# Optimization experiments

Measured on AMD Instinct MI355X. Metric: run time of the kernel, lower is better.

Reference implementation:

```python
import jax, jax.numpy as jnp
import numpy as np

NUM_HEADS = 16
HEAD_SIZE = 64
D_MODEL = NUM_HEADS * HEAD_SIZE  # 1024


def setup_inputs() -> dict:
    key = jax.random.key(0)
    k_in, k_ctx, k_q, k_k, k_v, k_o, k_b = jax.random.split(key, 7)
    B, Sq, Skv, D = 4, 2048, 2048, D_MODEL
    inputs = jax.random.normal(k_in, (B, Sq, D), dtype=jnp.float32)
    context = jax.random.normal(k_ctx, (B, Skv, D), dtype=jnp.float32)
    s = 0.02
    Wq = jax.random.normal(k_q, (D, D), dtype=jnp.float32) * s
    Wk = jax.random.normal(k_k, (D, D), dtype=jnp.float32) * s
    Wv = jax.random.normal(k_v, (D, D), dtype=jnp.float32) * s
    Wo = jax.random.normal(k_o, (D, D), dtype=jnp.float32) * s
    bo = jnp.zeros((D,), dtype=jnp.float32)
    return {"inputs": inputs, "context": context, "Wq": Wq, "Wk": Wk,
            "Wv": Wv, "Wo": Wo, "bo": bo}


def reference(inputs, context, Wq, Wk, Wv, Wo, bo):
    # inputs: [B, Sq, D]; context: [B, Skv, D]
    B, Sq, _ = inputs.shape
    H, Dh = NUM_HEADS, HEAD_SIZE
    scale = Dh ** -0.5
    q = (inputs @ Wq).reshape(B, Sq, H, Dh)          # [B,Sq,H,Dh]
    k = (context @ Wk).reshape(B, -1, H, Dh)          # [B,Skv,H,Dh]
    v = (context @ Wv).reshape(B, -1, H, Dh)
    # The chunked online-softmax recurrence in the source is exactly softmax attention.
    scores = jnp.einsum('bqhd,bkhd->bhqk', q, k) * scale
    probs = jax.nn.softmax(scores, axis=-1)
    attn = jnp.einsum('bhqk,bkhd->bqhd', probs, v)    # [B,Sq,H,Dh]
    out = attn.reshape(B, Sq, H * Dh)
    return out @ Wo + bo
```

## Files before the change

kernel.cpp:

```cpp
#include <hip/hip_runtime.h>
#include <hip/hip_bf16.h>


#define D_MODEL 1024
#define NHEAD   16
#define DHEAD   64
#define BATCH   4
#define SEQ     2048
#define MROWS   (BATCH * SEQ)
#define WP      ((size_t)D_MODEL * D_MODEL)

typedef unsigned short u16;
typedef __attribute__((ext_vector_type(8))) _Float16       f16x8;
typedef __attribute__((ext_vector_type(2))) _Float16       f16x2;
typedef __attribute__((ext_vector_type(4))) float          f32x4;
typedef __attribute__((ext_vector_type(8))) unsigned short u16x8;
typedef __attribute__((ext_vector_type(4))) unsigned short u16x4;

__device__ __forceinline__ u16 f2h(float x) {
    union { _Float16 h; u16 u; } cv;
    cv.h = (_Float16)x;
    return cv.u;
}

__device__ __forceinline__ unsigned pkrtz(float a, float b) {
    unsigned r;
    asm("v_cvt_pkrtz_f16_f32 %0, %1, %2" : "=v"(r) : "v"(a), "v"(b));
    return r;
}

__device__ __forceinline__ f32x4 mfma16h(f16x8 a, f16x8 b, f32x4 c) {
    return __builtin_amdgcn_mfma_f32_16x16x32_f16(a, b, c, 0, 0, 0);
}

__device__ __forceinline__ float exp2fast(float x) {
    float r;
    asm("v_exp_f32 %0, %1" : "=v"(r) : "v"(x));
    return r;
}

__device__ __forceinline__ void glds16(const void* g, void* l) {
    __builtin_amdgcn_global_load_lds(
        (const __attribute__((address_space(1))) void*)g,
        (__attribute__((address_space(3))) void*)l, 16, 0, 0);
}

__global__ __launch_bounds__(256) void cvt16(const float* __restrict__ a,
                                             const float* __restrict__ b,
                                             u16* __restrict__ oa,
                                             u16* __restrict__ ob) {
    const size_t i = ((size_t)blockIdx.x * 256 + threadIdx.x) * 8;
    {
        float4 v0 = *(const float4*)(a + i);
        float4 v1 = *(const float4*)(a + i + 4);
        u16x8 h;
        h[0] = f2h(v0.x); h[1] = f2h(v0.y); h[2] = f2h(v0.z); h[3] = f2h(v0.w);
        h[4] = f2h(v1.x); h[5] = f2h(v1.y); h[6] = f2h(v1.z); h[7] = f2h(v1.w);
        *(u16x8*)(oa + i) = h;
    }
    {
        float4 v0 = *(const float4*)(b + i);
        float4 v1 = *(const float4*)(b + i + 4);
        u16x8 h;
        h[0] = f2h(v0.x); h[1] = f2h(v0.y); h[2] = f2h(v0.z); h[3] = f2h(v0.w);
        h[4] = f2h(v1.x); h[5] = f2h(v1.y); h[6] = f2h(v1.z); h[7] = f2h(v1.w);
        *(u16x8*)(ob + i) = h;
    }
}

__global__ __launch_bounds__(256) void wtransh(const float* __restrict__ W0,
                                               const float* __restrict__ W1,
                                               const float* __restrict__ W2,
                                               const float* __restrict__ W3,
                                               u16* __restrict__ wt, float qscale) {
    const int z = blockIdx.z;
    const float* W = (z == 0) ? W0 : (z == 1) ? W1 : (z == 2) ? W2 : W3;
    const float scale = (z == 2) ? qscale : 1.0f;
    u16* T = wt + (size_t)z * WP;

    const int k0 = blockIdx.x * 64, n0 = blockIdx.y * 64;
    const int t = threadIdx.x;
    __shared__ u16 th[64 * 64];
#pragma unroll
    for (int rep = 0; rep < 4; ++rep) {
        int kr = (t >> 4) + 16 * rep;
        int nc = (t & 15) * 4;
        float4 v = *(const float4*)(W + (size_t)(k0 + kr) * D_MODEL + n0 + nc);
#pragma unroll
        for (int u = 0; u < 4; ++u) {
            int n = nc + u;
            th[n * 64 + (kr ^ (8 * ((n >> 3) & 7)))] = f2h(((const float*)&v)[u] * scale);
        }
    }
    __syncthreads();
#pragma unroll
    for (int rep = 0; rep < 2; ++rep) {
        int n = (t >> 3) + 32 * rep;
        int kb = (t & 7) * 8;
        int a = n * 64 + (kb ^ (8 * ((n >> 3) & 7)));
        *(u16x8*)(T + (size_t)(n0 + n) * D_MODEL + k0 + kb) = *(const u16x8*)&th[a];
    }
}

__global__ __launch_bounds__(256) void gemm_proj(const u16* __restrict__ Actx,
                                                 const u16* __restrict__ Ainp,
                                                 const u16* __restrict__ Bh,
                                                 u16* __restrict__ Kf,
                                                 u16* __restrict__ Vimg,
                                                 u16* __restrict__ Qf) {
    const int K = 1024;
    __shared__ u16 sA[128 * 32];
    __shared__ u16 sB[128 * 32];

    const int t = threadIdx.x;
    const int w = t >> 6, l = t & 63, g = l >> 4, lr = l & 15;
    const int wrow = (w >> 1) * 64, wcol = (w & 1) * 64;

    const int bid = blockIdx.x;
    const int vg = bid >> 9;
    const int inner = bid & 511;
    const int wgs = (inner & 7) * 64 + (inner >> 3);
    const int bm = wgs >> 3, bn8 = wgs & 7;
    const int bn = vg * 8 + bn8;

    const u16* A16 = (vg < 2) ? Actx : Ainp;

    f32x4 acc[4][4];
#pragma unroll
    for (int i = 0; i < 4; ++i)
#pragma unroll
        for (int j = 0; j < 4; ++j) acc[i][j] = (f32x4){0.f, 0.f, 0.f, 0.f};

    const int srow = t >> 2;
    const int scg  = (t & 3) * 8;

    for (int k0 = 0; k0 < K; k0 += 32) {
#pragma unroll
        for (int rep = 0; rep < 2; ++rep) {
            const int row  = srow + 64 * rep;
            const int lofs = row * 32 + scg;
            glds16(A16 + (size_t)(bm * 128 + row) * K + k0 + scg, &sA[lofs]);
            glds16(Bh  + (size_t)(bn * 128 + row) * K + k0 + scg, &sB[lofs]);
        }
        __syncthreads();

        f16x8 a[4], b[4];
#pragma unroll
        for (int f = 0; f < 4; ++f) {
            a[f] = *(const f16x8*)&sA[(wrow + f * 16 + lr) * 32 + 8 * g];
            b[f] = *(const f16x8*)&sB[(wcol + f * 16 + lr) * 32 + 8 * g];
        }
        __builtin_amdgcn_s_setprio(1);
#pragma unroll
        for (int fi = 0; fi < 4; ++fi)
#pragma unroll
            for (int fj = 0; fj < 4; ++fj)
                acc[fi][fj] = mfma16h(a[fi], b[fj], acc[fi][fj]);
        __builtin_amdgcn_s_setprio(0);
        __syncthreads();
    }

    if (vg == 0) {
#pragma unroll
        for (int fj = 0; fj < 4; ++fj) {
            const int colg = bn8 * 128 + wcol + fj * 16 + lr;
#pragma unroll
            for (int fi = 0; fi < 4; ++fi) {
                const int rowb = bm * 128 + wrow + fi * 16 + 4 * g;
#pragma unroll
                for (int j = 0; j < 4; ++j)
                    Kf[(size_t)(rowb + j) * D_MODEL + colg] = f2h(acc[fi][fj][j]);
            }
        }
    } else if (vg == 1) {
        const int rowb0 = bm * 128 + wrow;
        const int bidx = rowb0 >> 11;
        const int tile = (rowb0 & 2047) >> 6;
#pragma unroll
        for (int fj = 0; fj < 4; ++fj) {
            const int vcol = bn8 * 128 + wcol + fj * 16 + lr;
            const int vh = vcol >> 6, vd = vcol & 63;
            const size_t tbase = ((size_t)((bidx * NHEAD + vh) * 32) + tile) * 4096;
            const int dsw = vd & 7;
#pragma unroll
            for (int fi = 0; fi < 4; ++fi) {
                const int qp = g | ((fi >> 1) << 2);
                const int i0 = (fi & 1) << 2;
                const int q  = qp ^ dsw;
                u16x4 hv;
#pragma unroll
                for (int j = 0; j < 4; ++j) hv[j] = f2h(acc[fi][fj][j]);
                *(u16x4*)(Vimg + tbase + vd * 64 + 8 * q + i0) = hv;
            }
        }
    } else {
#pragma unroll
        for (int fj = 0; fj < 4; ++fj) {
            const int colg = bn8 * 128 + wcol + fj * 16 + lr;
#pragma unroll
            for (int fi = 0; fi < 4; ++fi) {
                const int rowb = bm * 128 + wrow + fi * 16 + 4 * g;
#pragma unroll
                for (int j = 0; j < 4; ++j)
                    Qf[(size_t)(rowb + j) * D_MODEL + colg] = f2h(acc[fi][fj][j]);
            }
        }
    }
}

__global__ __launch_bounds__(256) void gemm_out(const u16* __restrict__ A16,
                                                const u16* __restrict__ Bh,
                                                const float* __restrict__ bias,
                                                float* __restrict__ Cf) {
    const int K = 1024, N = 1024;
    __shared__ u16 sA[64 * 32];
    __shared__ u16 sB[128 * 32];

    const int t = threadIdx.x;
    const int w = t >> 6, l = t & 63, g = l >> 4, lr = l & 15;
    const int wrow = (w >> 1) * 32, wcol = (w & 1) * 64;

    const int bid = blockIdx.x;
    const int wg = (bid & 7) * 128 + (bid >> 3);
    const int bm = wg & 127, bn = wg >> 7;

    f32x4 acc[2][4];
#pragma unroll
    for (int i = 0; i < 2; ++i)
#pragma unroll
        for (int j = 0; j < 4; ++j) acc[i][j] = (f32x4){0.f, 0.f, 0.f, 0.f};

    const int srow = t >> 2;
    const int scg  = (t & 3) * 8;

    for (int k0 = 0; k0 < K; k0 += 32) {
        glds16(A16 + (size_t)(bm * 64 + srow) * K + k0 + scg, &sA[srow * 32 + scg]);
#pragma unroll
        for (int rep = 0; rep < 2; ++rep) {
            const int row = srow + 64 * rep;
            glds16(Bh + (size_t)(bn * 128 + row) * K + k0 + scg, &sB[row * 32 + scg]);
        }
        __syncthreads();

        f16x8 a[2], b[4];
#pragma unroll
        for (int f = 0; f < 2; ++f)
            a[f] = *(const f16x8*)&sA[(wrow + f * 16 + lr) * 32 + 8 * g];
#pragma unroll
        for (int f = 0; f < 4; ++f)
            b[f] = *(const f16x8*)&sB[(wcol + f * 16 + lr) * 32 + 8 * g];
        __builtin_amdgcn_s_setprio(1);
#pragma unroll
        for (int fi = 0; fi < 2; ++fi)
#pragma unroll
            for (int fj = 0; fj < 4; ++fj)
                acc[fi][fj] = mfma16h(a[fi], b[fj], acc[fi][fj]);
        __builtin_amdgcn_s_setprio(0);
        __syncthreads();
    }

#pragma unroll
    for (int fj = 0; fj < 4; ++fj) {
        const int colg = bn * 128 + wcol + fj * 16 + lr;
        const float bv = bias[colg];
#pragma unroll
        for (int fi = 0; fi < 2; ++fi) {
            const int rowb = bm * 64 + wrow + fi * 16 + 4 * g;
#pragma unroll
            for (int j = 0; j < 4; ++j)
                Cf[(size_t)(rowb + j) * N + colg] = acc[fi][fj][j] + bv;
        }
    }
}

__global__ __launch_bounds__(512) void attn_mfma9(const u16* __restrict__ Qf,
                                                  const u16* __restrict__ Kf,
                                                  const u16* __restrict__ Vimg,
                                                  u16* __restrict__ Af16) {
    const int bid = blockIdx.x;
    const int wg = (bid & 7) * 128 + (bid >> 3);
    const int qt = wg & 15;
    const int hb = wg >> 4;
    const int h = hb & 15, b = hb >> 4;

    const int t = threadIdx.x, w = t >> 6, l = t & 63, g = l >> 4, lr = l & 15;

    __shared__ u16 Ks[2][4096];
    __shared__ u16 Vs[2][4096];

    const size_t qb = (size_t)(b * SEQ + qt * 128 + w * 16 + lr) * D_MODEL + h * DHEAD;
    f16x8 qf0 = *(const f16x8*)(Qf + qb + 8 * g);
    f16x8 qf1 = *(const f16x8*)(Qf + qb + 32 + 8 * g);

    f32x4 o[4];
#pragma unroll
    for (int c = 0; c < 4; ++c) o[c] = (f32x4){0.f, 0.f, 0.f, 0.f};
    float lsum = 0.f;

    const u16* Kh = Kf + (size_t)(b * SEQ) * D_MODEL + h * DHEAD;
    const size_t vtb = (size_t)((b * NHEAD + h) * 32) * 4096;

    const int kr_ = t >> 3, kd0 = (t & 7) * 8;
    const int ksrc  = kd0 ^ ((kr_ & 7) << 3);
    const int klofs = t * 8;
    const int kkey  = (lr & 7) << 3;

    const f16x2 ones2 = {(_Float16)1.0f, (_Float16)1.0f};

    auto stage = [&](int bb, int kv0) {
        glds16(Kh + (size_t)(kv0 + kr_) * D_MODEL + ksrc, &Ks[bb][klofs]);
        glds16(Vimg + vtb + (size_t)(kv0 >> 6) * 4096 + (size_t)t * 8, &Vs[bb][klofs]);
    };

    stage(0, 0);

    for (int it = 0; it < SEQ / 64; ++it) {
        const int cb = it & 1;
        __syncthreads();
        if (it < SEQ / 64 - 1) stage(cb ^ 1, (it + 1) << 6);

        f32x4 s[4];
#pragma unroll
        for (int rt = 0; rt < 4; ++rt) s[rt] = (f32x4){-4.f, -4.f, -4.f, -4.f};
        __builtin_amdgcn_s_setprio(1);
#pragma unroll
        for (int rt = 0; rt < 4; ++rt) {
            const int rb = (16 * rt + lr) * 64;
            f16x8 k80 = *(const f16x8*)&Ks[cb][rb + ((8 * g) ^ kkey)];
            f16x8 k81 = *(const f16x8*)&Ks[cb][rb + ((8 * g + 32) ^ kkey)];
            s[rt] = mfma16h(k80, qf0, s[rt]);
            s[rt] = mfma16h(k81, qf1, s[rt]);
        }
        __builtin_amdgcn_s_setprio(0);

#pragma unroll
        for (int rt = 0; rt < 4; ++rt)
#pragma unroll
            for (int j = 0; j < 4; ++j)
                s[rt][j] = exp2fast(s[rt][j]);

        float rs = 0.f;
        f16x8 pbq[2];
#pragma unroll
        for (int ks = 0; ks < 2; ++ks) {
            union { unsigned w[4]; f16x8 v; } pk;
#pragma unroll
            for (int pr = 0; pr < 4; ++pr) {
                const int rt = 2 * ks + (pr >> 1);
                const int j0 = (pr & 1) * 2;
                const unsigned pw = pkrtz(s[rt][j0], s[rt][j0 + 1]);
                pk.w[pr] = pw;
                union { unsigned w; f16x2 h2; } cv;
                cv.w = pw;
                rs = __builtin_amdgcn_fdot2(cv.h2, ones2, rs, false);
            }
            pbq[ks] = pk.v;
        }
        lsum += rs;

        __builtin_amdgcn_s_setprio(1);
#pragma unroll
        for (int ks = 0; ks < 2; ++ks)
#pragma unroll
            for (int c = 0; c < 4; ++c) {
                const int dv = 16 * c + lr;
                f16x8 v8 = *(const f16x8*)&Vs[cb][dv * 64 + ((8 * g + 32 * ks) ^ ((dv & 7) << 3))];
                o[c] = mfma16h(v8, pbq[ks], o[c]);
            }
        __builtin_amdgcn_s_setprio(0);
    }

    lsum += __shfl_xor(lsum, 16);
    lsum += __shfl_xor(lsum, 32);
    const float inv = 1.f / lsum;
    u16* op = Af16 + qb;
#pragma unroll
    for (int c = 0; c < 4; ++c) {
        u16x4 hv;
#pragma unroll
        for (int j = 0; j < 4; ++j) hv[j] = f2h(o[c][j] * inv);
        *(u16x4*)(op + 16 * c + 4 * g) = hv;
    }
}

extern "C" void kernel_launch(void* const* d_in, const int* in_sizes, int n_in,
                              void* d_out, int out_size, void* d_ws, size_t ws_size,
                              hipStream_t stream) {
    const float* inputs  = (const float*)d_in[0];
    const float* context = (const float*)d_in[1];
    const float* Wq      = (const float*)d_in[2];
    const float* Wk      = (const float*)d_in[3];
    const float* Wv      = (const float*)d_in[4];
    const float* Wo      = (const float*)d_in[5];
    const float* bo      = (const float*)d_in[6];
    float* out = (float*)d_out;

    const size_t P = (size_t)MROWS * D_MODEL;

    u16* base  = (u16*)d_ws;
    u16* ctx16 = base;
    u16* in16  = base + P;
    u16* kf    = base + 2 * P;
    u16* vimg  = base + 3 * P;
    u16* qf    = base + 4 * P;
    u16* af    = base + 5 * P;
    u16* wt    = base + 6 * P;
    u16* woh   = wt + 3 * WP;

    const float QSCALE = 0.18033688011112042f;

    cvt16<<<dim3(P / (256 * 8)), dim3(256), 0, stream>>>(context, inputs, ctx16, in16);

    wtransh<<<dim3(16, 16, 4), dim3(256), 0, stream>>>(Wk, Wv, Wq, Wo, wt, QSCALE);

    gemm_proj<<<dim3(1536), dim3(256), 0, stream>>>(ctx16, in16, wt, kf, vimg, qf);

    attn_mfma9<<<dim3(1024), dim3(512), 0, stream>>>(qf, kf, vimg, af);

    gemm_out<<<dim3(1024), dim3(256), 0, stream>>>(af, woh, bo, out);
}
```

Measured before the change: 241.7 us.

## Pipeline attention QK and softmax-PV across tiles, double query rows per wave

After: 250.7 us. 1.04x slower.

```diff
diff --git a/kernel.cpp b/kernel.cpp
--- a/kernel.cpp
+++ b/kernel.cpp
@@ -45,42 +45,48 @@
         (__attribute__((address_space(3))) void*)l, 16, 0, 0);
 }
 
-__global__ __launch_bounds__(256) void cvt16(const float* __restrict__ a,
-                                             const float* __restrict__ b,
-                                             u16* __restrict__ oa,
-                                             u16* __restrict__ ob) {
-    const size_t i = ((size_t)blockIdx.x * 256 + threadIdx.x) * 8;
-    {
-        float4 v0 = *(const float4*)(a + i);
-        float4 v1 = *(const float4*)(a + i + 4);
-        u16x8 h;
-        h[0] = f2h(v0.x); h[1] = f2h(v0.y); h[2] = f2h(v0.z); h[3] = f2h(v0.w);
-        h[4] = f2h(v1.x); h[5] = f2h(v1.y); h[6] = f2h(v1.z); h[7] = f2h(v1.w);
-        *(u16x8*)(oa + i) = h;
-    }
-    {
-        float4 v0 = *(const float4*)(b + i);
-        float4 v1 = *(const float4*)(b + i + 4);
-        u16x8 h;
-        h[0] = f2h(v0.x); h[1] = f2h(v0.y); h[2] = f2h(v0.z); h[3] = f2h(v0.w);
-        h[4] = f2h(v1.x); h[5] = f2h(v1.y); h[6] = f2h(v1.z); h[7] = f2h(v1.w);
-        *(u16x8*)(ob + i) = h;
-    }
-}
-
-__global__ __launch_bounds__(256) void wtransh(const float* __restrict__ W0,
-                                               const float* __restrict__ W1,
-                                               const float* __restrict__ W2,
-                                               const float* __restrict__ W3,
-                                               u16* __restrict__ wt, float qscale) {
-    const int z = blockIdx.z;
+__global__ __launch_bounds__(256) void prep(const float* __restrict__ ctx,
+                                            const float* __restrict__ inp,
+                                            u16* __restrict__ ctx16,
+                                            u16* __restrict__ in16,
+                                            const float* __restrict__ W0,
+                                            const float* __restrict__ W1,
+                                            const float* __restrict__ W2,
+                                            const float* __restrict__ W3,
+                                            u16* __restrict__ wt, float qscale) {
+    __shared__ u16 th[64 * 64];
+    const int id = blockIdx.x;
+    const int t = threadIdx.x;
+
+    if (id < 4096) {
+        const size_t i = ((size_t)id * 256 + t) * 8;
+        {
+            float4 v0 = *(const float4*)(ctx + i);
+            float4 v1 = *(const float4*)(ctx + i + 4);
+            u16x8 h;
+            h[0] = f2h(v0.x); h[1] = f2h(v0.y); h[2] = f2h(v0.z); h[3] = f2h(v0.w);
+            h[4] = f2h(v1.x); h[5] = f2h(v1.y); h[6] = f2h(v1.z); h[7] = f2h(v1.w);
+            *(u16x8*)(ctx16 + i) = h;
+        }
+        {
+            float4 v0 = *(const float4*)(inp + i);
+            float4 v1 = *(const float4*)(inp + i + 4);
+            u16x8 h;
+            h[0] = f2h(v0.x); h[1] = f2h(v0.y); h[2] = f2h(v0.z); h[3] = f2h(v0.w);
+            h[4] = f2h(v1.x); h[5] = f2h(v1.y); h[6] = f2h(v1.z); h[7] = f2h(v1.w);
+            *(u16x8*)(in16 + i) = h;
+        }
+        return;
+    }
+
+    const int id2 = id - 4096;
+    const int z = id2 >> 8;
+    const int rem = id2 & 255;
     const float* W = (z == 0) ? W0 : (z == 1) ? W1 : (z == 2) ? W2 : W3;
     const float scale = (z == 2) ? qscale : 1.0f;
     u16* T = wt + (size_t)z * WP;
-
-    const int k0 = blockIdx.x * 64, n0 = blockIdx.y * 64;
-    const int t = threadIdx.x;
-    __shared__ u16 th[64 * 64];
+    const int k0 = (rem & 15) * 64, n0 = (rem >> 4) * 64;
+
 #pragma unroll
     for (int rep = 0; rep < 4; ++rep) {
         int kr = (t >> 4) + 16 * rep;
@@ -273,29 +279,36 @@
     }
 }
 
-__global__ __launch_bounds__(512) void attn_mfma9(const u16* __restrict__ Qf,
-                                                  const u16* __restrict__ Kf,
-                                                  const u16* __restrict__ Vimg,
-                                                  u16* __restrict__ Af16) {
+__global__ __launch_bounds__(512, 4) void attn_mfma10(const u16* __restrict__ Qf,
+                                                      const u16* __restrict__ Kf,
+                                                      const u16* __restrict__ Vimg,
+                                                      u16* __restrict__ Af16) {
     const int bid = blockIdx.x;
-    const int wg = (bid & 7) * 128 + (bid >> 3);
-    const int qt = wg & 15;
-    const int hb = wg >> 4;
+    const int wg = (bid & 7) * 64 + (bid >> 3);
+    const int qt = wg & 7;
+    const int hb = wg >> 3;
     const int h = hb & 15, b = hb >> 4;
 
     const int t = threadIdx.x, w = t >> 6, l = t & 63, g = l >> 4, lr = l & 15;
 
     __shared__ u16 Ks[2][4096];
-    __shared__ u16 Vs[2][4096];
-
-    const size_t qb = (size_t)(b * SEQ + qt * 128 + w * 16 + lr) * D_MODEL + h * DHEAD;
-    f16x8 qf0 = *(const f16x8*)(Qf + qb + 8 * g);
-    f16x8 qf1 = *(const f16x8*)(Qf + qb + 32 + 8 * g);
-
-    f32x4 o[4];
-#pragma unroll
-    for (int c = 0; c < 4; ++c) o[c] = (f32x4){0.f, 0.f, 0.f, 0.f};
-    float lsum = 0.f;
+    __shared__ u16 Vs[4][4096];
+
+    f16x8 qf[2][2];
+#pragma unroll
+    for (int qg = 0; qg < 2; ++qg) {
+        const size_t qb = (size_t)(b * SEQ + qt * 256 + w * 32 + qg * 16 + lr) * D_MODEL + h * DHEAD;
+#pragma unroll
+        for (int c = 0; c < 2; ++c)
+            qf[qg][c] = *(const f16x8*)(Qf + qb + 32 * c + 8 * g);
+    }
+
+    f32x4 o[2][4];
+#pragma unroll
+    for (int qg = 0; qg < 2; ++qg)
+#pragma unroll
+        for (int c = 0; c < 4; ++c) o[qg][c] = (f32x4){0.f, 0.f, 0.f, 0.f};
+    float lsum[2] = {0.f, 0.f};
 
     const u16* Kh = Kf + (size_t)(b * SEQ) * D_MODEL + h * DHEAD;
     const size_t vtb = (size_t)((b * NHEAD + h) * 32) * 4096;
@@ -307,79 +320,109 @@
 
     const f16x2 ones2 = {(_Float16)1.0f, (_Float16)1.0f};
 
-    auto stage = [&](int bb, int kv0) {
-        glds16(Kh + (size_t)(kv0 + kr_) * D_MODEL + ksrc, &Ks[bb][klofs]);
-        glds16(Vimg + vtb + (size_t)(kv0 >> 6) * 4096 + (size_t)t * 8, &Vs[bb][klofs]);
+    auto stage = [&](int tile) {
+        glds16(Kh + (size_t)((tile << 6) + kr_) * D_MODEL + ksrc, &Ks[tile & 1][klofs]);
+        glds16(Vimg + vtb + (size_t)tile * 4096 + (size_t)t * 8, &Vs[tile & 3][klofs]);
     };
 
-    stage(0, 0);
-
-    for (int it = 0; it < SEQ / 64; ++it) {
-        const int cb = it & 1;
-        __syncthreads();
-        if (it < SEQ / 64 - 1) stage(cb ^ 1, (it + 1) << 6);
-
-        f32x4 s[4];
-#pragma unroll
-        for (int rt = 0; rt < 4; ++rt) s[rt] = (f32x4){-4.f, -4.f, -4.f, -4.f};
+    auto qk = [&](const u16* Kbuf, f32x4 (&s)[2][4]) {
+#pragma unroll
+        for (int qg = 0; qg < 2; ++qg)
+#pragma unroll
+            for (int rt = 0; rt < 4; ++rt) s[qg][rt] = (f32x4){-4.f, -4.f, -4.f, -4.f};
         __builtin_amdgcn_s_setprio(1);
 #pragma unroll
         for (int rt = 0; rt < 4; ++rt) {
             const int rb = (16 * rt + lr) * 64;
-            f16x8 k80 = *(const f16x8*)&Ks[cb][rb + ((8 * g) ^ kkey)];
-            f16x8 k81 = *(const f16x8*)&Ks[cb][rb + ((8 * g + 32) ^ kkey)];
-            s[rt] = mfma16h(k80, qf0, s[rt]);
-            s[rt] = mfma16h(k81, qf1, s[rt]);
+#pragma unroll
+            for (int c = 0; c < 2; ++c) {
+                f16x8 k8 = *(const f16x8*)&Kbuf[rb + ((8 * g + 32 * c) ^ kkey)];
+#pragma unroll
+                for (int qg = 0; qg < 2; ++qg)
+                    s[qg][rt] = mfma16h(k8, qf[qg][c], s[qg][rt]);
+            }
         }
         __builtin_amdgcn_s_setprio(0);
-
-#pragma unroll
-        for (int rt = 0; rt < 4; ++rt)
-#pragma unroll
-            for (int j = 0; j < 4; ++j)
-                s[rt][j] = exp2fast(s[rt][j]);
-
-        float rs = 0.f;
-        f16x8 pbq[2];
-#pragma unroll
-        for (int ks = 0; ks < 2; ++ks) {
-            union { unsigned w[4]; f16x8 v; } pk;
-#pragma unroll
-            for (int pr = 0; pr < 4; ++pr) {
-                const int rt = 2 * ks + (pr >> 1);
-                const int j0 = (pr & 1) * 2;
-                const unsigned pw = pkrtz(s[rt][j0], s[rt][j0 + 1]);
-                pk.w[pr] = pw;
-                union { unsigned w; f16x2 h2; } cv;
-                cv.w = pw;
-                rs = __builtin_amdgcn_fdot2(cv.h2, ones2, rs, false);
+    };
+
+    auto smpv = [&](f32x4 (&s)[2][4], const u16* Vbuf) {
+#pragma unroll
+        for (int qg = 0; qg < 2; ++qg) {
+#pragma unroll
+            for (int rt = 0; rt < 4; ++rt)
+#pragma unroll
+                for (int j = 0; j < 4; ++j)
+                    s[qg][rt][j] = exp2fast(s[qg][rt][j]);
+
+            float rs = 0.f;
+            f16x8 pbq[2];
+#pragma unroll
+            for (int ks = 0; ks < 2; ++ks) {
+                union { unsigned w_[4]; f16x8 v; } pk;
+#pragma unroll
+                for (int pr = 0; pr < 4; ++pr) {
+                    const int rt = 2 * ks + (pr >> 1);
+                    const int j0 = (pr & 1) * 2;
+                    const unsigned pw = pkrtz(s[qg][rt][j0], s[qg][rt][j0 + 1]);
+                    pk.w_[pr] = pw;
+                    union { unsigned w_; f16x2 h2; } cv;
+                    cv.w_ = pw;
+                    rs = __builtin_amdgcn_fdot2(cv.h2, ones2, rs, false);
+                }
+                pbq[ks] = pk.v;
             }
-            pbq[ks] = pk.v;
-        }
-        lsum += rs;
-
-        __builtin_amdgcn_s_setprio(1);
-#pragma unroll
-        for (int ks = 0; ks < 2; ++ks)
-#pragma unroll
-            for (int c = 0; c < 4; ++c) {
-                const int dv = 16 * c + lr;
-                f16x8 v8 = *(const f16x8*)&Vs[cb][dv * 64 + ((8 * g + 32 * ks) ^ ((dv & 7) << 3))];
-                o[c] = mfma16h(v8, pbq[ks], o[c]);
-            }
-        __builtin_amdgcn_s_setprio(0);
-    }
-
-    lsum += __shfl_xor(lsum, 16);
-    lsum += __shfl_xor(lsum, 32);
-    const float inv = 1.f / lsum;
-    u16* op = Af16 + qb;
-#pragma unroll
-    for (int c = 0; c < 4; ++c) {
-        u16x4 hv;
-#pragma unroll
-        for (int j = 0; j < 4; ++j) hv[j] = f2h(o[c][j] * inv);
-        *(u16x4*)(op + 16 * c + 4 * g) = hv;
+            lsum[qg] += rs;
+
+            __builtin_amdgcn_s_setprio(1);
+#pragma unroll
+            for (int ks = 0; ks < 2; ++ks)
+#pragma unroll
+                for (int c = 0; c < 4; ++c) {
+                    const int dv = 16 * c + lr;
+                    f16x8 v8 = *(const f16x8*)&Vbuf[dv * 64 + ((8 * g + 32 * ks) ^ ((dv & 7) << 3))];
+                    o[qg][c] = mfma16h(v8, pbq[ks], o[qg][c]);
+                }
+            __builtin_amdgcn_s_setprio(0);
+        }
+    };
+
+    f32x4 sA[2][4], sB[2][4];
+
+    stage(0);
+    __syncthreads();
+    stage(1);
+    qk(Ks[0], sA);
+    __syncthreads();
+
+    for (int oo = 0; oo < 15; ++oo) {
+        const int i1 = 2 * oo + 1, i2 = 2 * oo + 2;
+        stage(i1 + 1);
+        qk(Ks[1], sB);
+        smpv(sA, Vs[(i1 - 1) & 3]);
+        __syncthreads();
+        stage(i2 + 1);
+        qk(Ks[0], sA);
+        smpv(sB, Vs[(i2 - 1) & 3]);
+        __syncthreads();
+    }
+
+    qk(Ks[1], sB);
+    smpv(sA, Vs[2]);
+    smpv(sB, Vs[3]);
+
+#pragma unroll
+    for (int qg = 0; qg < 2; ++qg) {
+        lsum[qg] += __shfl_xor(lsum[qg], 16);
+        lsum[qg] += __shfl_xor(lsum[qg], 32);
+        const float inv = 1.f / lsum[qg];
+        u16* op = Af16 + (size_t)(b * SEQ + qt * 256 + w * 32 + qg * 16 + lr) * D_MODEL + h * DHEAD;
+#pragma unroll
+        for (int c = 0; c < 4; ++c) {
+            u16x4 hv;
+#pragma unroll
+            for (int j = 0; j < 4; ++j) hv[j] = f2h(o[qg][c][j] * inv);
+            *(u16x4*)(op + 16 * c + 4 * g) = hv;
+        }
     }
 }
 
@@ -409,13 +452,12 @@
 
     const float QSCALE = 0.18033688011112042f;
 
-    cvt16<<<dim3(P / (256 * 8)), dim3(256), 0, stream>>>(context, inputs, ctx16, in16);
-
-    wtransh<<<dim3(16, 16, 4), dim3(256), 0, stream>>>(Wk, Wv, Wq, Wo, wt, QSCALE);
+    prep<<<dim3(5120), dim3(256), 0, stream>>>(context, inputs, ctx16, in16,
+                                               Wk, Wv, Wq, Wo, wt, QSCALE);
 
     gemm_proj<<<dim3(1536), dim3(256), 0, stream>>>(ctx16, in16, wt, kf, vimg, qf);
 
-    attn_mfma9<<<dim3(1024), dim3(512), 0, stream>>>(qf, kf, vimg, af);
+    attn_mfma10<<<dim3(512), dim3(512), 0, stream>>>(qf, kf, vimg, af);
 
     gemm_out<<<dim3(1024), dim3(256), 0, stream>>>(af, woh, bo, out);
 }
```
